# Kernel tuning notes

Hardware: AMD Instinct MI355X
Metric: run time of the kernel (lower is better)

Reference implementation:

```python
import jax, jax.numpy as jnp
import numpy as np

NUM_HEADS = 8
QK_DIM = 64
V_DIM = 64


def _conv1x1(W, b, x):
    # W: [out, in], x: [N, in, T, V] -> [N, out, T, V]
    return jnp.einsum('oc,nctv->notv', W, x) + b[None, :, None, None]


def setup_inputs() -> dict:
    key = jax.random.key(0)
    ks = jax.random.split(key, 10)
    N, C, T, V = 8, 256, 1024, 25
    s = 0.02
    return {
        'feature': jax.random.normal(ks[0], (N, C, T, V), jnp.float32),
        'text_feature': jax.random.normal(ks[1], (1, 512, 1, V), jnp.float32),
        'Wq': jax.random.normal(ks[2], (NUM_HEADS * QK_DIM, 512), jnp.float32) * s,
        'bq': jax.random.normal(ks[3], (NUM_HEADS * QK_DIM,), jnp.float32) * s,
        'Wk': jax.random.normal(ks[4], (NUM_HEADS * QK_DIM, 512), jnp.float32) * s,
        'bk': jax.random.normal(ks[5], (NUM_HEADS * QK_DIM,), jnp.float32) * s,
        'Wv': jax.random.normal(ks[6], (V_DIM, C), jnp.float32) * s,
        'bv': jax.random.normal(ks[7], (V_DIM,), jnp.float32) * s,
        'Wo': jax.random.normal(ks[8], (C, NUM_HEADS * V_DIM), jnp.float32) * s,
        'bo': jax.random.normal(ks[9], (C,), jnp.float32) * s,
    }


def reference(feature, text_feature, Wq, bq, Wk, bk, Wv, bv, Wo, bo):
    N, C, T, V = feature.shape
    tf = jnp.broadcast_to(text_feature, (N, 512, 1, V))  # expand over batch
    # Q/K from text features (T dim collapses to 1)
    q = _conv1x1(Wq, bq, tf).reshape(N, NUM_HEADS, QK_DIM, V)
    k = _conv1x1(Wk, bk, tf).reshape(N, NUM_HEADS, QK_DIM, V)
    v = _conv1x1(Wv, bv, feature)  # [N, v_dim, T, V]
    energy = jnp.einsum('nhcu,nhcv->nhuv', q, k) / jnp.sqrt(jnp.float32(QK_DIM))
    attn = jax.nn.softmax(energy, axis=-1)  # [N, H, V, V]
    z = jnp.einsum('nctu,nhuv->nhctv', v, attn).reshape(N, NUM_HEADS * V_DIM, T, V)
    out = _conv1x1(Wo, bo, z) + feature
    return out
```

## Files before the change

### kernel.cpp

```cpp
#include <hip/hip_runtime.h>
#include <hip/hip_bf16.h>


typedef __attribute__((ext_vector_type(8))) short short8;
typedef __attribute__((ext_vector_type(4))) short short4v;
typedef __attribute__((ext_vector_type(4))) float f4v;

static __device__ __forceinline__ unsigned short f2bf(float f) {
  union { float f; unsigned u; } v; v.f = f;
  unsigned r = v.u + 0x7fffu + ((v.u >> 16) & 1u);
  return (unsigned short)(r >> 16);
}
static __device__ __forceinline__ float bf2f(unsigned short h) {
  union { unsigned u; float f; } v; v.u = ((unsigned)h) << 16;
  return v.f;
}


__global__ void k_qk_conv(const float* __restrict__ tf,
                          const float* __restrict__ Wq, const float* __restrict__ bq,
                          const float* __restrict__ Wk, const float* __restrict__ bk,
                          const float* __restrict__ Wv, const float* __restrict__ Wo,
                          unsigned short* __restrict__ WvP,
                          unsigned short* __restrict__ WoP,
                          float* __restrict__ qkP)
{
  __shared__ float tfl[12800];
  const int b = blockIdx.x, tid = threadIdx.x;
  if (b < 100) {
    for (int i = tid; i < 12800; i += 256) tfl[i] = tf[i];
    __syncthreads();
    int idx = b * 256 + tid;
    int isK = idx >= 12800;
    int j = isK ? idx - 12800 : idx;
    int g = j / 25, u = j - 25 * g;
    const float* wrow = (isK ? Wk : Wq) + g * 512;
    float s = (isK ? bk : bq)[g];
    for (int i = 0; i < 512; ++i) s += wrow[i] * tfl[i * 25 + u];
    qkP[idx] = s;
  } else {
    int cb = b - 100;
    for (int i = cb * 256 + tid; i < 16384; i += 64 * 256) {
      WvP[i] = f2bf(Wv[i]);
    }
    for (int i = cb * 256 + tid; i < 131072; i += 64 * 256) {
      WoP[i] = f2bf(Wo[i]);
    }
  }
}

__global__ void k_attn(const float* __restrict__ qkP,
                       unsigned short* __restrict__ attnP)
{
  __shared__ float ql[1600], kl[1600], attl[625];
  const int h = blockIdx.x, tid = threadIdx.x;
  for (int i = tid; i < 1600; i += 256) {
    ql[i] = qkP[h * 1600 + i];
    kl[i] = qkP[12800 + h * 1600 + i];
  }
  __syncthreads();
  if (tid < 25) {
    int u = tid;
    float e[25];
    float mx = -1e30f;
    #pragma unroll
    for (int v = 0; v < 25; ++v) {
      float s = 0.f;
      #pragma unroll
      for (int r = 0; r < 64; ++r) s += ql[r * 25 + u] * kl[r * 25 + v];
      s *= 0.125f;
      e[v] = s;
      mx = fmaxf(mx, s);
    }
    float den = 0.f;
    #pragma unroll
    for (int v = 0; v < 25; ++v) { e[v] = __expf(e[v] - mx); den += e[v]; }
    float inv = 1.f / den;
    #pragma unroll
    for (int v = 0; v < 25; ++v) attl[u * 25 + v] = e[v] * inv;
  }
  __syncthreads();
  for (int i = tid; i < 1280; i += 256) {
    int vp = i / 40, u = i - 40 * vp;
    attnP[h * 1280 + i] =
        (vp < 25 && u < 25) ? f2bf(attl[u * 25 + vp]) : (unsigned short)0;
  }
}

__launch_bounds__(512)
__attribute__((amdgpu_waves_per_eu(2, 2)))
__global__ void k_main(const float* __restrict__ feature,
                       const float* __restrict__ bv,
                       const float* __restrict__ bo,
                       const unsigned short* __restrict__ WvP,
                       const unsigned short* __restrict__ WoP,
                       const unsigned short* __restrict__ attnP,
                       float* __restrict__ out)
{
  extern __shared__ char smem[];
  unsigned short* FlA = (unsigned short*)smem;
  unsigned short* FlB = (unsigned short*)(smem + 33792);
  unsigned short* Vl  = (unsigned short*)(smem + 67584);
  unsigned short* Zl  = (unsigned short*)(smem + 76800);

  const int tid  = threadIdx.x;
  const int wave = tid >> 6;
  const int lane = tid & 63;
  const int quad = lane >> 4;
  const int l16  = lane & 15;
  const int wg    = blockIdx.x;
  const int n     = wg & 7;
  const int chunk = wg >> 3;

  const int c = tid >> 1, p = tid & 1;
  const size_t rowbase = ((size_t)(n * 256 + c) * 1024) * 25;

  short8 wo[2][16];
  #pragma unroll
  for (int mi = 0; mi < 2; ++mi)
    #pragma unroll
    for (int ks = 0; ks < 16; ++ks)
      wo[mi][ks] = *reinterpret_cast<const short8*>(
          WoP + (wave * 32 + mi * 16 + l16) * 512 + ks * 32 + quad * 8);

  const int mt1 = wave & 3, nh1 = wave >> 2;
  short8 wa[8];
  #pragma unroll
  for (int ks = 0; ks < 8; ++ks)
    wa[ks] = *reinterpret_cast<const short8*>(
        WvP + (mt1 * 16 + l16) * 256 + ks * 32 + quad * 8);

  const int t2 = wave >> 2, q2 = wave & 3;
  short8 ab[4];
  #pragma unroll
  for (int nj = 0; nj < 4; ++nj) {
    int h = 2 * q2 + (nj >> 1), vph = nj & 1;
    ab[nj] = *reinterpret_cast<const short8*>(
        attnP + h * 1280 + (vph * 16 + l16) * 40 + quad * 8);
  }

  float bo4[2][4];
  #pragma unroll
  for (int mi = 0; mi < 2; ++mi)
    #pragma unroll
    for (int r = 0; r < 4; ++r) bo4[mi][r] = bo[wave * 32 + mi * 16 + quad * 4 + r];
  float bvv[4];
  #pragma unroll
  for (int r = 0; r < 4; ++r) bvv[r] = bv[mt1 * 16 + quad * 4 + r];

  {
    short8 z = {0, 0, 0, 0, 0, 0, 0, 0};
    for (int i = tid; i < 924; i += 512) {
      int pc = i / 33, off = i - 33 * pc;
      unsigned short* F = (pc < 14) ? FlA : FlB;
      int r = (pc < 14) ? pc : pc - 14;
      int t = r / 7, vp = 25 + (r - 7 * t);
      *reinterpret_cast<short8*>(&F[(t * 32 + vp) * 264 + off * 8]) = z;
    }
  }

  {
    float2 f0[13];
    const float2* s2 = reinterpret_cast<const float2*>(
        feature + rowbase + (size_t)(chunk * 32) * 25);
    #pragma unroll
    for (int j = 0; j < 13; ++j) { int i = p + 2 * j; if (i < 25) f0[j] = s2[i]; }
    #pragma unroll
    for (int j = 0; j < 13; ++j) {
      int i = p + 2 * j;
      if (i < 25) {
        int j0 = 2 * i;
        { int jj = j0;     int t = (jj >= 25); int vp = jj - 25 * t; FlA[(t*32+vp)*264 + c] = f2bf(f0[j].x); }
        { int jj = j0 + 1; int t = (jj >= 25); int vp = jj - 25 * t; FlA[(t*32+vp)*264 + c] = f2bf(f0[j].y); }
      }
    }
  }
  __syncthreads();

  #pragma unroll 1
  for (int it = 0; it < 16; ++it) {
    unsigned short* Fc  = (it & 1) ? FlB : FlA;
    unsigned short* Fnx = (it & 1) ? FlA : FlB;
    const int t0 = chunk * 32 + it * 2;

    float2 fn[13];
    if (it < 15) {
      const float2* s2 = reinterpret_cast<const float2*>(
          feature + rowbase + (size_t)(t0 + 2) * 25);
      #pragma unroll
      for (int j = 0; j < 13; ++j) { int i = p + 2 * j; if (i < 25) fn[j] = s2[i]; }
      __builtin_amdgcn_sched_barrier(0);
    }

    {
      f4v accv[2];
      #pragma unroll
      for (int ni = 0; ni < 2; ++ni)
        #pragma unroll
        for (int r = 0; r < 4; ++r) accv[ni][r] = bvv[r];
      #pragma unroll
      for (int ks = 0; ks < 8; ++ks) {
        #pragma unroll
        for (int ni = 0; ni < 2; ++ni) {
          int colb = (2 * nh1 + ni) * 16 + l16;
          short8 b = *reinterpret_cast<const short8*>(&Fc[colb * 264 + ks * 32 + quad * 8]);
          accv[ni] = __builtin_amdgcn_mfma_f32_16x16x32_bf16(wa[ks], b, accv[ni], 0, 0, 0);
        }
      }
      #pragma unroll
      for (int ni = 0; ni < 2; ++ni) {
        int colb = (2 * nh1 + ni) * 16 + l16;
        #pragma unroll
        for (int r = 0; r < 4; ++r) {
          int cc = mt1 * 16 + quad * 4 + r;
          Vl[cc * 72 + colb] = f2bf(accv[ni][r]);
        }
      }
    }

    if (it < 15) {
      #pragma unroll
      for (int j = 0; j < 13; ++j) {
        int i = p + 2 * j;
        if (i < 25) {
          int j0 = 2 * i;
          { int jj = j0;     int t = (jj >= 25); int vp = jj - 25 * t; Fnx[(t*32+vp)*264 + c] = f2bf(fn[j].x); }
          { int jj = j0 + 1; int t = (jj >= 25); int vp = jj - 25 * t; Fnx[(t*32+vp)*264 + c] = f2bf(fn[j].y); }
        }
      }
    }

    f4v acc[2][4];
    #pragma unroll
    for (int mi = 0; mi < 2; ++mi) {
      const int o0 = wave * 32 + mi * 16 + quad * 4;
      #pragma unroll
      for (int ni = 0; ni < 4; ++ni) {
        short4v fr = *reinterpret_cast<const short4v*>(&Fc[(ni * 16 + l16) * 264 + o0]);
        #pragma unroll
        for (int r = 0; r < 4; ++r)
          acc[mi][ni][r] = bo4[mi][r] + bf2f((unsigned short)fr[r]);
      }
    }
    __syncthreads();

    #pragma unroll
    for (int mi = 0; mi < 4; ++mi) {
      short8 a = *reinterpret_cast<const short8*>(
          &Vl[(mi * 16 + l16) * 72 + t2 * 32 + quad * 8]);
      #pragma unroll
      for (int nj = 0; nj < 4; ++nj) {
        f4v z = {0.f, 0.f, 0.f, 0.f};
        f4v az = __builtin_amdgcn_mfma_f32_16x16x32_bf16(a, ab[nj], z, 0, 0, 0);
        int h = 2 * q2 + (nj >> 1), vph = nj & 1;
        int col = t2 * 32 + vph * 16 + l16;
        int k0 = h * 64 + mi * 16 + quad * 4;
        short4v zz;
        #pragma unroll
        for (int r = 0; r < 4; ++r) zz[r] = (short)f2bf(az[r]);
        *reinterpret_cast<short4v*>(&Zl[col * 520 + k0]) = zz;
      }
    }
    __syncthreads();

    #pragma unroll
    for (int ks = 0; ks < 16; ++ks) {
      #pragma unroll
      for (int ni = 0; ni < 4; ++ni) {
        short8 bfr = *reinterpret_cast<const short8*>(
            &Zl[(ni * 16 + l16) * 520 + ks * 32 + quad * 8]);
        #pragma unroll
        for (int mi = 0; mi < 2; ++mi)
          acc[mi][ni] =
              __builtin_amdgcn_mfma_f32_16x16x32_bf16(wo[mi][ks], bfr, acc[mi][ni], 0, 0, 0);
      }
    }

    #pragma unroll
    for (int ni = 0; ni < 4; ++ni) {
      int colb = ni * 16 + l16;
      int t = colb >> 5, vp = colb & 31;
      if (vp < 25) {
        #pragma unroll
        for (int mi = 0; mi < 2; ++mi)
          #pragma unroll
          for (int r = 0; r < 4; ++r) {
            int o = wave * 32 + mi * 16 + quad * 4 + r;
            out[((size_t)(n * 256 + o) * 1024 + (t0 + t)) * 25 + vp] = acc[mi][ni][r];
          }
      }
    }
  }
}

extern "C" void kernel_launch(void* const* d_in, const int* in_sizes, int n_in,
                              void* d_out, int out_size, void* d_ws, size_t ws_size,
                              hipStream_t stream)
{
  const float* feature = (const float*)d_in[0];
  const float* tf      = (const float*)d_in[1];
  const float* Wq      = (const float*)d_in[2];
  const float* bq      = (const float*)d_in[3];
  const float* Wk      = (const float*)d_in[4];
  const float* bk      = (const float*)d_in[5];
  const float* Wv      = (const float*)d_in[6];
  const float* bv      = (const float*)d_in[7];
  const float* Wo      = (const float*)d_in[8];
  const float* bo      = (const float*)d_in[9];
  float* out = (float*)d_out;

  unsigned short* WvP   = (unsigned short*)d_ws;
  unsigned short* WoP   = WvP + 16384;
  unsigned short* attnP = WoP + 131072;
  float* qkP = (float*)(attnP + 10240);

  hipLaunchKernelGGL(k_qk_conv, dim3(164), dim3(256), 0, stream,
                     tf, Wq, bq, Wk, bk, Wv, Wo, WvP, WoP, qkP);
  hipLaunchKernelGGL(k_attn, dim3(8), dim3(256), 0, stream, qkP, attnP);

  hipFuncSetAttribute(reinterpret_cast<const void*>(&k_main),
                      hipFuncAttributeMaxDynamicSharedMemorySize, 143360);
  hipLaunchKernelGGL(k_main, dim3(256), dim3(512), 143360, stream,
                     feature, bv, bo, WvP, WoP, attnP, out);
}
```

Measured before the change: 530.7 us.

## Stream weights from global, shrink LDS, swizzle tiles, double grid for occupancy

Measured after the change: 962.3 us. 81.3% more time.

```diff
diff --git a/kernel.cpp b/kernel.cpp
--- a/kernel.cpp
+++ b/kernel.cpp
@@ -87,8 +87,7 @@
   }
 }
 
-__launch_bounds__(512)
-__attribute__((amdgpu_waves_per_eu(2, 2)))
+__launch_bounds__(512, 4)
 __global__ void k_main(const float* __restrict__ feature,
                        const float* __restrict__ bv,
                        const float* __restrict__ bo,
@@ -98,10 +97,9 @@
                        float* __restrict__ out)
 {
   extern __shared__ char smem[];
-  unsigned short* FlA = (unsigned short*)smem;
-  unsigned short* FlB = (unsigned short*)(smem + 33792);
-  unsigned short* Vl  = (unsigned short*)(smem + 67584);
-  unsigned short* Zl  = (unsigned short*)(smem + 76800);
+  unsigned short* Fl = (unsigned short*)smem;
+  unsigned short* Vl = (unsigned short*)(smem + 33792);
+  unsigned short* Zl = (unsigned short*)(smem + 43008);
 
   const int tid  = threadIdx.x;
   const int wave = tid >> 6;
@@ -115,29 +113,16 @@
   const int c = tid >> 1, p = tid & 1;
   const size_t rowbase = ((size_t)(n * 256 + c) * 1024) * 25;
 
-  short8 wo[2][16];
+  const int mt1 = wave & 3, nh1 = wave >> 2;
+  const int hl  = wave & 3;
+  const int mig = (wave >> 2) * 2;
+  short8 ab[2][2];
   #pragma unroll
-  for (int mi = 0; mi < 2; ++mi)
-    #pragma unroll
-    for (int ks = 0; ks < 16; ++ks)
-      wo[mi][ks] = *reinterpret_cast<const short8*>(
-          WoP + (wave * 32 + mi * 16 + l16) * 512 + ks * 32 + quad * 8);
-
-  const int mt1 = wave & 3, nh1 = wave >> 2;
-  short8 wa[8];
-  #pragma unroll
-  for (int ks = 0; ks < 8; ++ks)
-    wa[ks] = *reinterpret_cast<const short8*>(
-        WvP + (mt1 * 16 + l16) * 256 + ks * 32 + quad * 8);
-
-  const int t2 = wave >> 2, q2 = wave & 3;
-  short8 ab[4];
-  #pragma unroll
-  for (int nj = 0; nj < 4; ++nj) {
-    int h = 2 * q2 + (nj >> 1), vph = nj & 1;
-    ab[nj] = *reinterpret_cast<const short8*>(
-        attnP + h * 1280 + (vph * 16 + l16) * 40 + quad * 8);
-  }
+  for (int H = 0; H < 2; ++H)
+    #pragma unroll
+    for (int vph = 0; vph < 2; ++vph)
+      ab[H][vph] = *reinterpret_cast<const short8*>(
+          attnP + (H * 4 + hl) * 1280 + (vph * 16 + l16) * 40 + quad * 8);
 
   float bo4[2][4];
   #pragma unroll
@@ -148,21 +133,22 @@
   #pragma unroll
   for (int r = 0; r < 4; ++r) bvv[r] = bv[mt1 * 16 + quad * 4 + r];
 
+  const unsigned short* wob = WoP + (wave * 32 + l16) * 512 + quad * 8;
+  const unsigned short* wvb = WvP + (mt1 * 16 + l16) * 256 + quad * 8;
+
   {
     short8 z = {0, 0, 0, 0, 0, 0, 0, 0};
-    for (int i = tid; i < 924; i += 512) {
-      int pc = i / 33, off = i - 33 * pc;
-      unsigned short* F = (pc < 14) ? FlA : FlB;
-      int r = (pc < 14) ? pc : pc - 14;
-      int t = r / 7, vp = 25 + (r - 7 * t);
-      *reinterpret_cast<short8*>(&F[(t * 32 + vp) * 264 + off * 8]) = z;
+    for (int i = tid; i < 448; i += 512) {
+      int pc = i >> 5, off = i & 31;
+      int t = pc / 7, vp = 25 + (pc - 7 * t);
+      *reinterpret_cast<short8*>(&Fl[(t * 32 + vp) * 264 + off * 8]) = z;
     }
   }
 
   {
     float2 f0[13];
     const float2* s2 = reinterpret_cast<const float2*>(
-        feature + rowbase + (size_t)(chunk * 32) * 25);
+        feature + rowbase + (size_t)(chunk * 16) * 25);
     #pragma unroll
     for (int j = 0; j < 13; ++j) { int i = p + 2 * j; if (i < 25) f0[j] = s2[i]; }
     #pragma unroll
@@ -170,21 +156,21 @@
       int i = p + 2 * j;
       if (i < 25) {
         int j0 = 2 * i;
-        { int jj = j0;     int t = (jj >= 25); int vp = jj - 25 * t; FlA[(t*32+vp)*264 + c] = f2bf(f0[j].x); }
-        { int jj = j0 + 1; int t = (jj >= 25); int vp = jj - 25 * t; FlA[(t*32+vp)*264 + c] = f2bf(f0[j].y); }
+        { int jj = j0;     int t = (jj >= 25); int vp = jj - 25 * t; int col = t*32+vp;
+          Fl[col * 264 + (c ^ ((col & 7) << 3))] = f2bf(f0[j].x); }
+        { int jj = j0 + 1; int t = (jj >= 25); int vp = jj - 25 * t; int col = t*32+vp;
+          Fl[col * 264 + (c ^ ((col & 7) << 3))] = f2bf(f0[j].y); }
       }
     }
   }
   __syncthreads();
 
   #pragma unroll 1
-  for (int it = 0; it < 16; ++it) {
-    unsigned short* Fc  = (it & 1) ? FlB : FlA;
-    unsigned short* Fnx = (it & 1) ? FlA : FlB;
-    const int t0 = chunk * 32 + it * 2;
+  for (int it = 0; it < 8; ++it) {
+    const int t0 = chunk * 16 + it * 2;
 
     float2 fn[13];
-    if (it < 15) {
+    if (it < 7) {
       const float2* s2 = reinterpret_cast<const float2*>(
           feature + rowbase + (size_t)(t0 + 2) * 25);
       #pragma unroll
@@ -198,13 +184,20 @@
       for (int ni = 0; ni < 2; ++ni)
         #pragma unroll
         for (int r = 0; r < 4; ++r) accv[ni][r] = bvv[r];
+      short8 wap[2];
+      wap[0] = *reinterpret_cast<const short8*>(wvb);
+      wap[1] = *reinterpret_cast<const short8*>(wvb + 32);
       #pragma unroll
       for (int ks = 0; ks < 8; ++ks) {
+        short8 a = wap[ks & 1];
+        if (ks < 6)
+          wap[ks & 1] = *reinterpret_cast<const short8*>(wvb + (ks + 2) * 32);
         #pragma unroll
         for (int ni = 0; ni < 2; ++ni) {
           int colb = (2 * nh1 + ni) * 16 + l16;
-          short8 b = *reinterpret_cast<const short8*>(&Fc[colb * 264 + ks * 32 + quad * 8]);
-          accv[ni] = __builtin_amdgcn_mfma_f32_16x16x32_bf16(wa[ks], b, accv[ni], 0, 0, 0);
+          short8 b = *reinterpret_cast<const short8*>(
+              &Fl[colb * 264 + ((ks * 32 + quad * 8) ^ ((l16 & 7) << 3))]);
+          accv[ni] = __builtin_amdgcn_mfma_f32_16x16x32_bf16(a, b, accv[ni], 0, 0, 0);
         }
       }
       #pragma unroll
@@ -213,67 +206,93 @@
         #pragma unroll
         for (int r = 0; r < 4; ++r) {
           int cc = mt1 * 16 + quad * 4 + r;
-          Vl[cc * 72 + colb] = f2bf(accv[ni][r]);
-        }
-      }
-    }
-
-    if (it < 15) {
+          Vl[cc * 72 + (colb ^ ((cc & 7) << 3))] = f2bf(accv[ni][r]);
+        }
+      }
+    }
+
+    f4v acc[2][4];
+    #pragma unroll
+    for (int mi = 0; mi < 2; ++mi) {
+      const int o0 = wave * 32 + mi * 16 + quad * 4;
+      #pragma unroll
+      for (int ni = 0; ni < 4; ++ni) {
+        int colb = ni * 16 + l16;
+        short4v fr = *reinterpret_cast<const short4v*>(
+            &Fl[colb * 264 + (o0 ^ ((l16 & 7) << 3))]);
+        #pragma unroll
+        for (int r = 0; r < 4; ++r)
+          acc[mi][ni][r] = bo4[mi][r] + bf2f((unsigned short)fr[r]);
+      }
+    }
+    __syncthreads();
+
+    if (it < 7) {
       #pragma unroll
       for (int j = 0; j < 13; ++j) {
         int i = p + 2 * j;
         if (i < 25) {
           int j0 = 2 * i;
-          { int jj = j0;     int t = (jj >= 25); int vp = jj - 25 * t; Fnx[(t*32+vp)*264 + c] = f2bf(fn[j].x); }
-          { int jj = j0 + 1; int t = (jj >= 25); int vp = jj - 25 * t; Fnx[(t*32+vp)*264 + c] = f2bf(fn[j].y); }
-        }
-      }
-    }
-
-    f4v acc[2][4];
-    #pragma unroll
-    for (int mi = 0; mi < 2; ++mi) {
-      const int o0 = wave * 32 + mi * 16 + quad * 4;
-      #pragma unroll
-      for (int ni = 0; ni < 4; ++ni) {
-        short4v fr = *reinterpret_cast<const short4v*>(&Fc[(ni * 16 + l16) * 264 + o0]);
-        #pragma unroll
-        for (int r = 0; r < 4; ++r)
-          acc[mi][ni][r] = bo4[mi][r] + bf2f((unsigned short)fr[r]);
-      }
-    }
-    __syncthreads();
-
-    #pragma unroll
-    for (int mi = 0; mi < 4; ++mi) {
-      short8 a = *reinterpret_cast<const short8*>(
-          &Vl[(mi * 16 + l16) * 72 + t2 * 32 + quad * 8]);
-      #pragma unroll
-      for (int nj = 0; nj < 4; ++nj) {
-        f4v z = {0.f, 0.f, 0.f, 0.f};
-        f4v az = __builtin_amdgcn_mfma_f32_16x16x32_bf16(a, ab[nj], z, 0, 0, 0);
-        int h = 2 * q2 + (nj >> 1), vph = nj & 1;
-        int col = t2 * 32 + vph * 16 + l16;
-        int k0 = h * 64 + mi * 16 + quad * 4;
-        short4v zz;
-        #pragma unroll
-        for (int r = 0; r < 4; ++r) zz[r] = (short)f2bf(az[r]);
-        *reinterpret_cast<short4v*>(&Zl[col * 520 + k0]) = zz;
-      }
-    }
-    __syncthreads();
-
-    #pragma unroll
-    for (int ks = 0; ks < 16; ++ks) {
-      #pragma unroll
-      for (int ni = 0; ni < 4; ++ni) {
-        short8 bfr = *reinterpret_cast<const short8*>(
-            &Zl[(ni * 16 + l16) * 520 + ks * 32 + quad * 8]);
-        #pragma unroll
-        for (int mi = 0; mi < 2; ++mi)
-          acc[mi][ni] =
-              __builtin_amdgcn_mfma_f32_16x16x32_bf16(wo[mi][ks], bfr, acc[mi][ni], 0, 0, 0);
-      }
+          { int jj = j0;     int t = (jj >= 25); int vp = jj - 25 * t; int col = t*32+vp;
+            Fl[col * 264 + (c ^ ((col & 7) << 3))] = f2bf(fn[j].x); }
+          { int jj = j0 + 1; int t = (jj >= 25); int vp = jj - 25 * t; int col = t*32+vp;
+            Fl[col * 264 + (c ^ ((col & 7) << 3))] = f2bf(fn[j].y); }
+        }
+      }
+    }
+
+    #pragma unroll
+    for (int H = 0; H < 2; ++H) {
+      #pragma unroll
+      for (int mo = 0; mo < 2; ++mo) {
+        const int mi2 = mig + mo;
+        #pragma unroll
+        for (int t = 0; t < 2; ++t) {
+          const int row = mi2 * 16 + l16;
+          short8 a = *reinterpret_cast<const short8*>(
+              &Vl[row * 72 + ((t * 32 + quad * 8) ^ ((l16 & 7) << 3))]);
+          #pragma unroll
+          for (int vph = 0; vph < 2; ++vph) {
+            f4v z = {0.f, 0.f, 0.f, 0.f};
+            f4v az = __builtin_amdgcn_mfma_f32_16x16x32_bf16(a, ab[H][vph], z, 0, 0, 0);
+            int col = t * 32 + vph * 16 + l16;
+            int k0 = hl * 64 + mi2 * 16 + quad * 4;
+            short4v zz;
+            #pragma unroll
+            for (int r = 0; r < 4; ++r) zz[r] = (short)f2bf(az[r]);
+            *reinterpret_cast<short4v*>(
+                &Zl[col * 264 + (k0 ^ ((col & 7) << 3))]) = zz;
+          }
+        }
+      }
+      __syncthreads();
+
+      {
+        const unsigned short* wb = wob + H * 256;
+        short8 wop[2][2];
+        wop[0][0] = *reinterpret_cast<const short8*>(wb);
+        wop[0][1] = *reinterpret_cast<const short8*>(wb + 8192);
+        wop[1][0] = *reinterpret_cast<const short8*>(wb + 32);
+        wop[1][1] = *reinterpret_cast<const short8*>(wb + 8192 + 32);
+        #pragma unroll
+        for (int ksl = 0; ksl < 8; ++ksl) {
+          short8 w0 = wop[ksl & 1][0];
+          short8 w1 = wop[ksl & 1][1];
+          if (ksl < 6) {
+            wop[ksl & 1][0] = *reinterpret_cast<const short8*>(wb + (ksl + 2) * 32);
+            wop[ksl & 1][1] = *reinterpret_cast<const short8*>(wb + 8192 + (ksl + 2) * 32);
+          }
+          #pragma unroll
+          for (int ni = 0; ni < 4; ++ni) {
+            int row = ni * 16 + l16;
+            short8 bfr = *reinterpret_cast<const short8*>(
+                &Zl[row * 264 + ((ksl * 32 + quad * 8) ^ ((l16 & 7) << 3))]);
+            acc[0][ni] = __builtin_amdgcn_mfma_f32_16x16x32_bf16(w0, bfr, acc[0][ni], 0, 0, 0);
+            acc[1][ni] = __builtin_amdgcn_mfma_f32_16x16x32_bf16(w1, bfr, acc[1][ni], 0, 0, 0);
+          }
+        }
+      }
+      __syncthreads();
     }
 
     #pragma unroll
@@ -319,7 +338,7 @@
   hipLaunchKernelGGL(k_attn, dim3(8), dim3(256), 0, stream, qkP, attnP);
 
   hipFuncSetAttribute(reinterpret_cast<const void*>(&k_main),
-                      hipFuncAttributeMaxDynamicSharedMemorySize, 143360);
-  hipLaunchKernelGGL(k_main, dim3(256), dim3(512), 143360, stream,
+                      hipFuncAttributeMaxDynamicSharedMemorySize, 76800);
+  hipLaunchKernelGGL(k_main, dim3(512), dim3(512), 76800, stream,
                      feature, bv, bo, WvP, WoP, attnP, out);
 }
```
